# Kernel optimization log

Hardware: AMD Instinct MI355X
Metric: run time of the kernel (lower is better)

The kernel has to match this reference:

```python
import jax, jax.numpy as jnp
import numpy as np

NUM_GROUPS = 4
DIVERSITY_STRENGTH = -0.5   # module stores -diversity_strength
DIVERSITY_DISCOUNT = 0.5
CAND_MULT = 1
N_GRAM = 2


def setup_inputs() -> dict:
    key = jax.random.key(0)
    k1, k2, k3, k5, k6 = jax.random.split(key, 5)
    bsz, beam, vocab, T = 64, 8, 50257, 128
    return {
        "lprobs": jax.random.normal(k1, (bsz, beam, vocab), jnp.float32),
        "scores": jax.random.normal(k2, (bsz, beam, T), jnp.float32),
        "group_overlap": jax.random.uniform(k3, (bsz, NUM_GROUPS, NUM_GROUPS), jnp.float32),
        "original_batch_idxs": jnp.arange(bsz, dtype=jnp.int32),
        "last_n_gram_indices": jax.random.randint(k5, (bsz, beam, N_GRAM - 1), 0, vocab, jnp.int32),
        "mask_last_n_gram_indices": jax.random.randint(k6, (bsz, beam, N_GRAM), 0, 2, jnp.int32),
        "step": 5,
    }


def reference(lprobs, scores, group_overlap, original_batch_idxs,
              last_n_gram_indices, mask_last_n_gram_indices, step):
    bsz, beam, vocab = lprobs.shape
    G = NUM_GROUPS
    mb = beam // G  # mini beam size
    k = CAND_MULT * mb
    batch_ar = jnp.arange(bsz)[:, None]

    scores_G, beams_G, idx_G = [], [], []
    for g in range(G):
        lp = lprobs[:, g::G, :]                       # [bsz, mb, vocab]
        sc = scores[:, g::G, step - 1]                # [bsz, mb]
        mk = mask_last_n_gram_indices[:, g::G, :]     # [bsz, mb, n_gram]
        if g > 0:
            # diversity penalty: scatter-add (1 + overlap) at previously picked tokens
            pen = 1.0 + group_overlap[original_batch_idxs, g, :g]          # [bsz, g]
            src = jnp.broadcast_to(pen[:, None, :], (bsz, mb, g)).reshape(bsz, -1)
            prev_idx = jnp.stack(idx_G, axis=-1).reshape(bsz, -1)          # [bsz, mb*g]
            div = jnp.zeros((bsz, vocab), lp.dtype).at[batch_ar, prev_idx].add(src)
            lp = lp + DIVERSITY_STRENGTH * div[:, None, :]
        # n-gram overlap mask: zero out beams whose mask rows are not all ones
        valid = (mk.sum(-1) == N_GRAM)                # [bsz, mb]
        lp = jnp.where(valid[:, :, None], lp, 0.0)
        # step > 0: add accumulated beam scores
        lp = lp + sc[:, :, None]
        flat = lp.reshape(bsz, -1)                    # [bsz, mb*vocab]
        top_idx = jax.lax.top_k(flat, k)[1]
        top_val = jnp.take_along_axis(flat, top_idx, axis=-1)
        beams_G.append((top_idx // vocab) * G + g)
        idx_G.append(top_idx % vocab)
        scores_G.append(top_val)

    scores_buf = jnp.stack(scores_G, axis=2).reshape(bsz, -1)   # [bsz, beam]
    indices_buf = jnp.stack(idx_G, axis=2).reshape(bsz, -1)
    beams_buf = jnp.stack(beams_G, axis=2).reshape(bsz, -1)

    # Hamming-cumulative overlap: [bsz, beam, n_gram] present n-grams, grouped
    present = jnp.concatenate(
        [last_n_gram_indices, indices_buf[:, :, None]], axis=-1
    ).reshape(bsz, mb, G, N_GRAM)
    eq = (present[:, :, None, :, :] == present[:, :, :, None, :])  # [bsz, mb, G, G, n]
    m = (mask_last_n_gram_indices != 0).reshape(bsz, mb, G, N_GRAM)
    om = m[:, :, None, :, :] & m[:, :, :, None, :]
    eq = jnp.where(om, eq, False)
    ov = (eq.sum(-1) == N_GRAM).astype(jnp.int32).sum(1)           # [bsz, G, G]

    new_group_overlap = (
        group_overlap.at[original_batch_idxs].add(ov.astype(group_overlap.dtype))
        * DIVERSITY_DISCOUNT
    )
    return scores_buf, indices_buf, beams_buf, new_group_overlap
```

## Files before the change

kernel.cpp:

```cpp
#include <hip/hip_runtime.h>
#include <math.h>

#define VOCAB 50257
#define BSZ   64
#define BEAM  8
#define NG    4
#define MB    2
#define KC    2
#define TLEN  128
#define NGRAM 2
#define SEG    64
#define SEGLEN 786
#define ROWS  (BSZ * BEAM)
#define MAXK  8
#define CAPQ  256

__device__ __forceinline__ bool better(float v1, int i1, float v2, int i2) {
    return (v1 > v2) || (v1 == v2 && i1 < i2);
}

struct Top2 { float v1, v2; int i1, i2; };

__device__ __forceinline__ void t2_init(Top2& t) {
    t.v1 = -INFINITY; t.v2 = -INFINITY; t.i1 = 0x7FFFFFFF; t.i2 = 0x7FFFFFFF;
}

__device__ __forceinline__ void t2_push(Top2& t, float v, int i) {
    if (better(v, i, t.v2, t.i2)) {
        if (better(v, i, t.v1, t.i1)) { t.v2 = t.v1; t.i2 = t.i1; t.v1 = v; t.i1 = i; }
        else                          { t.v2 = v;    t.i2 = i; }
    }
}

__device__ __forceinline__ void t2_merge(Top2& a, const Top2& b) {
    if (better(b.v1, b.i1, a.v1, a.i1)) {
        float nv2; int ni2;
        if (better(a.v1, a.i1, b.v2, b.i2)) { nv2 = a.v1; ni2 = a.i1; }
        else                                { nv2 = b.v2; ni2 = b.i2; }
        a.v1 = b.v1; a.i1 = b.i1; a.v2 = nv2; a.i2 = ni2;
    } else {
        if (better(b.v1, b.i1, a.v2, a.i2)) { a.v2 = b.v1; a.i2 = b.i1; }
    }
}

__device__ __forceinline__ float max4(float4 v) {
    return fmaxf(fmaxf(v.x, v.y), fmaxf(v.z, v.w));
}

__global__ __launch_bounds__(1024, 8) void dbs_candidates(
    const float* __restrict__ lprobs,
    const int*   __restrict__ mask,
    int*   __restrict__ meta,
    int*   __restrict__ wscnt,
    float* __restrict__ wscv,
    int*   __restrict__ wsci)
{
    const int tid  = threadIdx.x;
    const int w    = tid >> 6, lane = tid & 63;

    __shared__ unsigned long long s_bits[8];
    __shared__ float s_max[16];
    __shared__ float s_tau;
    __shared__ int   s_cnt;
    __shared__ float s_cv[CAPQ];
    __shared__ int   s_ci[CAPQ];

    bool validp = false;
    if (tid < ROWS) {
        const int2 mk = ((const int2*)mask)[tid];
        validp = (mk.x + mk.y) == NGRAM;
    }
    const unsigned long long bm = __ballot(validp);
    if (w < 8 && lane == 0) s_bits[w] = bm;
    if (tid == 0) s_cnt = 0;
    __syncthreads();

    int nv = 0;
    #pragma unroll
    for (int i = 0; i < 8; ++i) nv += __popcll(s_bits[i]);
    int k = 1;
    if (nv > 0) {
        const int q = ROWS / nv;
        k = (q >= 8) ? 8 : (q >= 4) ? 4 : (q >= 2) ? 2 : 1;
    }
    if (blockIdx.x == 0 && tid == 0) meta[0] = k;
    const int b = blockIdx.x;
    if (b >= nv * k) return;

    const int vidx  = b / k;
    const int slice = b - vidx * k;
    int r = 0, cnt = 0;
    for (int i = 0; i < 8; ++i) {
        const unsigned long long x = s_bits[i];
        const int c = __popcll(x);
        if (cnt + c > vidx) {
            unsigned long long y = x;
            for (int need = vidx - cnt; need > 0; --need) y &= y - 1;
            r = i * 64 + (__ffsll((unsigned long long)y) - 1);
            break;
        }
        cnt += c;
    }

    const size_t rowoff = (size_t)r * VOCAB;
    const float* row = lprobs + rowoff;

    const int segs = SEG / k;
    const int A    = slice * segs * SEGLEN;
    const int B    = min(A + segs * SEGLEN, VOCAB);
    const int L    = B - A;
    const int subL = (L + 15) >> 4;

    {
        const int start = A + w * subL;
        const int end   = min(start + subL, B);
        float m = -INFINITY;
        if (start < end) {
            const int mis = (int)((rowoff + start) & 3);
            int pre = (4 - mis) & 3;
            if (pre > end - start) pre = end - start;
            if (lane < pre) m = row[start + lane];
            const int vstart = start + pre;
            const int n4 = (end > vstart) ? ((end - vstart) >> 2) : 0;
            const float4* vrow = (const float4*)(row + vstart);

            float a0 = -INFINITY, a1 = -INFINITY, a2 = -INFINITY, a3 = -INFINITY;
            int jj = lane;
            for (; jj + 192 < n4; jj += 256) {
                a0 = fmaxf(a0, max4(vrow[jj]));
                a1 = fmaxf(a1, max4(vrow[jj + 64]));
                a2 = fmaxf(a2, max4(vrow[jj + 128]));
                a3 = fmaxf(a3, max4(vrow[jj + 192]));
            }
            for (; jj < n4; jj += 64) a0 = fmaxf(a0, max4(vrow[jj]));
            m = fmaxf(m, fmaxf(fmaxf(a0, a1), fmaxf(a2, a3)));
            const int tstart = vstart + 4 * n4;
            if (tstart + lane < end) m = fmaxf(m, row[tstart + lane]);
        }
        #pragma unroll
        for (int off = 32; off > 0; off >>= 1) m = fmaxf(m, __shfl_xor(m, off));
        if (lane == 0) s_max[w] = m;
    }
    __syncthreads();

    if (w == 0) {
        const float mym = (lane < 16) ? s_max[lane] : -INFINITY;
        int rank = 0;
        #pragma unroll
        for (int i = 0; i < 16; ++i) {
            const float om = __shfl(mym, i);
            rank += better(om, i, mym, lane) ? 1 : 0;
        }
        if (lane < 16 && rank == 7) s_tau = mym;
    }
    __syncthreads();
    const float tau = s_tau;

    if (s_max[w] >= tau) {
        const int start = A + w * subL;
        const int end   = min(start + subL, B);
        if (start < end) {
            const int mis = (int)((rowoff + start) & 3);
            int pre = (4 - mis) & 3;
            if (pre > end - start) pre = end - start;
            if (lane < pre) {
                const float v = row[start + lane];
                if (v >= tau) {
                    const int p = atomicAdd(&s_cnt, 1);
                    if (p < CAPQ) { s_cv[p] = v; s_ci[p] = start + lane; }
                }
            }
            const int vstart = start + pre;
            const int n4 = (end > vstart) ? ((end - vstart) >> 2) : 0;
            const float4* vrow = (const float4*)(row + vstart);

            for (int jj = lane; jj < n4; jj += 64) {
                const float4 v = vrow[jj];
                if (max4(v) >= tau) {
                    const int base = vstart + 4 * jj;
                    #pragma unroll
                    for (int e = 0; e < 4; ++e) {
                        const float ve = (e == 0) ? v.x : (e == 1) ? v.y
                                       : (e == 2) ? v.z : v.w;
                        if (ve >= tau) {
                            const int p = atomicAdd(&s_cnt, 1);
                            if (p < CAPQ) { s_cv[p] = ve; s_ci[p] = base + e; }
                        }
                    }
                }
            }
            const int tstart = vstart + 4 * n4;
            if (tstart + lane < end) {
                const float v = row[tstart + lane];
                if (v >= tau) {
                    const int p = atomicAdd(&s_cnt, 1);
                    if (p < CAPQ) { s_cv[p] = v; s_ci[p] = tstart + lane; }
                }
            }
        }
    }
    __syncthreads();

    const int ccnt = min(s_cnt, CAPQ);
    const int slot = r * MAXK + slice;
    if (tid == 0) wscnt[slot] = ccnt;
    for (int c = tid; c < ccnt; c += 1024) {
        wscv[(size_t)slot * CAPQ + c] = s_cv[c];
        wsci[(size_t)slot * CAPQ + c] = s_ci[c];
    }
}

__global__ __launch_bounds__(64) void dbs_final(
    const float* __restrict__ scores,
    const float* __restrict__ overlap,
    const int*   __restrict__ obi,
    const int*   __restrict__ lastn,
    const int*   __restrict__ mask,
    const int*   __restrict__ stepp,
    const int*   __restrict__ meta,
    const int*   __restrict__ wscnt,
    const float* __restrict__ wscv,
    const int*   __restrict__ wsci,
    float*       __restrict__ out)
{
    const int b   = blockIdx.x;
    const int tid = threadIdx.x;
    const int step = stepp[0];
    const int ob   = obi[b];

    __shared__ float s_sc[BEAM];
    __shared__ int   s_valid[BEAM];
    __shared__ int   s_k;
    __shared__ float s_pen[(NG-1)*KC];
    __shared__ int   s_penidx[(NG-1)*KC];
    __shared__ float s_selv[NG][KC];
    __shared__ int   s_seli[NG][KC];
    __shared__ int   s_selm[NG][KC];

    if (tid < BEAM) {
        const int* mk = mask + ((size_t)b * BEAM + tid) * NGRAM;
        s_valid[tid] = (mk[0] + mk[1]) == NGRAM;
        s_sc[tid]    = scores[((size_t)b * BEAM + tid) * TLEN + (step - 1)];
    }
    if (tid == 0) s_k = meta[0];
    __syncthreads();
    const int k = s_k;

    for (int g = 0; g < NG; ++g) {
        if (tid == 0) {
            for (int j = 0; j < g; ++j) {
                const float pen = 1.0f + overlap[((size_t)ob * NG + g) * NG + j];
                s_penidx[j*KC + 0] = s_seli[j][0]; s_pen[j*KC + 0] = pen;
                s_penidx[j*KC + 1] = s_seli[j][1]; s_pen[j*KC + 1] = pen;
            }
        }
        __syncthreads();

        const int np = KC * g;
        Top2 t; t2_init(t);
        for (int m = 0; m < MB; ++m) {
            const int beam = m * NG + g;
            if (s_valid[beam]) {
                const int r = b * BEAM + beam;
                for (int qq = 0; qq < k; ++qq) {
                    const int slot = r * MAXK + qq;
                    const int n = wscnt[slot];
                    for (int c = tid; c < n; c += 64) {
                        const float v   = wscv[(size_t)slot * CAPQ + c];
                        const int   idx = wsci[(size_t)slot * CAPQ + c];
                        float dv = 0.0f;
                        #pragma unroll
                        for (int p = 0; p < (NG-1)*KC; ++p)
                            if (p < np && s_penidx[p] == idx) dv += s_pen[p];
                        t2_push(t, v - 0.5f * dv + s_sc[beam], m * VOCAB + idx);
                    }
                }
            } else if (tid < KC) {
                t2_push(t, s_sc[beam], m * VOCAB + tid);
            }
        }

        #pragma unroll
        for (int off = 32; off > 0; off >>= 1) {
            Top2 o;
            o.v1 = __shfl_down(t.v1, off); o.i1 = __shfl_down(t.i1, off);
            o.v2 = __shfl_down(t.v2, off); o.i2 = __shfl_down(t.i2, off);
            t2_merge(t, o);
        }
        if (tid == 0) {
            s_selv[g][0] = t.v1; s_seli[g][0] = t.i1 % VOCAB; s_selm[g][0] = t.i1 / VOCAB;
            s_selv[g][1] = t.v2; s_seli[g][1] = t.i2 % VOCAB; s_selm[g][1] = t.i2 / VOCAB;
        }
        __syncthreads();
    }

    if (tid < KC * NG) {
        const int i = tid;
        const int m = i / NG, g = i % NG;
        out[(size_t)b * BEAM + i]        = s_selv[g][m];
        out[512 + (size_t)b * BEAM + i]  = (float)s_seli[g][m];
        out[1024 + (size_t)b * BEAM + i] = (float)(s_selm[g][m] * NG + g);
    }
    if (tid >= 16 && tid < 16 + NG * NG) {
        const int q  = tid - 16;
        const int g1 = q / NG, g2 = q % NG;
        int ov = 0;
        for (int m = 0; m < MB; ++m) {
            const int i1 = m * NG + g1, i2 = m * NG + g2;
            const int p1a = lastn[(size_t)b * BEAM + i1];
            const int p2a = lastn[(size_t)b * BEAM + i2];
            const int p1b = s_seli[g1][m];
            const int p2b = s_seli[g2][m];
            const int* mk1 = mask + ((size_t)b * BEAM + i1) * NGRAM;
            const int* mk2 = mask + ((size_t)b * BEAM + i2) * NGRAM;
            const bool e0 = (p1a == p2a) && (mk1[0] != 0) && (mk2[0] != 0);
            const bool e1 = (p1b == p2b) && (mk1[1] != 0) && (mk2[1] != 0);
            ov += (e0 && e1) ? 1 : 0;
        }
        out[1536 + (size_t)ob * (NG * NG) + q] =
            (overlap[(size_t)ob * (NG * NG) + q] + (float)ov) * 0.5f;
    }
}

extern "C" void kernel_launch(void* const* d_in, const int* in_sizes, int n_in,
                              void* d_out, int out_size, void* d_ws, size_t ws_size,
                              hipStream_t stream) {
    const float* lprobs  = (const float*)d_in[0];
    const float* scores  = (const float*)d_in[1];
    const float* overlap = (const float*)d_in[2];
    const int*   obi     = (const int*)d_in[3];
    const int*   lastn   = (const int*)d_in[4];
    const int*   mask    = (const int*)d_in[5];
    const int*   stepp   = (const int*)d_in[6];
    float*       out     = (float*)d_out;

    int*   meta  = (int*)d_ws;
    int*   wscnt = (int*)((char*)d_ws + 64);
    float* wscv  = (float*)((char*)d_ws + 64 + (size_t)ROWS * MAXK * 4);
    int*   wsci  = (int*)((char*)d_ws + 64 + (size_t)ROWS * MAXK * 4
                          + (size_t)ROWS * MAXK * CAPQ * 4);

    dbs_candidates<<<ROWS, 1024, 0, stream>>>(lprobs, mask, meta, wscnt, wscv, wsci);
    dbs_final     <<<BSZ, 64, 0, stream>>>(scores, overlap, obi, lastn, mask, stepp,
                                           meta, wscnt, wscv, wsci, out);
}
```

Baseline: 25.78 us.

## Fuse candidate scan and final selection into one cooperative kernel with grid sync

Folds the two kernels into one cooperative launch: every block runs the candidate scan, then a grid-wide barrier follows, and the first 64 blocks do the per-batch group top-2 selection and overlap update. If the cooperative launch fails, it falls back to the original two launches. The scan loop is also reshaped with fewer accumulators and an unconditional tail. This aims to remove the second launch gap, at the cost of grid-sync overhead and a residency requirement of 512 blocks of 1024 threads.

New measurement: 97.13 us. 3.77x slower.

```diff
diff --git a/kernel.cpp b/kernel.cpp
--- a/kernel.cpp
+++ b/kernel.cpp
@@ -1,4 +1,5 @@
 #include <hip/hip_runtime.h>
+#include <hip/hip_cooperative_groups.h>
 #include <math.h>
 
 #define VOCAB 50257
@@ -47,23 +48,14 @@
     return fmaxf(fmaxf(v.x, v.y), fmaxf(v.z, v.w));
 }
 
-__global__ __launch_bounds__(1024, 8) void dbs_candidates(
-    const float* __restrict__ lprobs,
-    const int*   __restrict__ mask,
-    int*   __restrict__ meta,
-    int*   __restrict__ wscnt,
-    float* __restrict__ wscv,
-    int*   __restrict__ wsci)
+__device__ __forceinline__ int scan_block(
+    const float* __restrict__ lprobs, const int* __restrict__ mask,
+    int* __restrict__ wscnt, float* __restrict__ wscv, int* __restrict__ wsci,
+    unsigned long long* s_bits, float* s_max, float* s_tau, int* s_cnt,
+    float* s_cv, int* s_ci)
 {
     const int tid  = threadIdx.x;
     const int w    = tid >> 6, lane = tid & 63;
-
-    __shared__ unsigned long long s_bits[8];
-    __shared__ float s_max[16];
-    __shared__ float s_tau;
-    __shared__ int   s_cnt;
-    __shared__ float s_cv[CAPQ];
-    __shared__ int   s_ci[CAPQ];
 
     bool validp = false;
     if (tid < ROWS) {
@@ -72,7 +64,7 @@
     }
     const unsigned long long bm = __ballot(validp);
     if (w < 8 && lane == 0) s_bits[w] = bm;
-    if (tid == 0) s_cnt = 0;
+    if (tid == 0) *s_cnt = 0;
     __syncthreads();
 
     int nv = 0;
@@ -83,9 +75,9 @@
         const int q = ROWS / nv;
         k = (q >= 8) ? 8 : (q >= 4) ? 4 : (q >= 2) ? 2 : 1;
     }
-    if (blockIdx.x == 0 && tid == 0) meta[0] = k;
+
     const int b = blockIdx.x;
-    if (b >= nv * k) return;
+    if (b >= nv * k) return k;
 
     const int vidx  = b / k;
     const int slice = b - vidx * k;
@@ -96,7 +88,7 @@
         if (cnt + c > vidx) {
             unsigned long long y = x;
             for (int need = vidx - cnt; need > 0; --need) y &= y - 1;
-            r = i * 64 + (__ffsll((unsigned long long)y) - 1);
+            r = i * 64 + (__ffsll(y) - 1);
             break;
         }
         cnt += c;
@@ -104,43 +96,43 @@
 
     const size_t rowoff = (size_t)r * VOCAB;
     const float* row = lprobs + rowoff;
-
     const int segs = SEG / k;
     const int A    = slice * segs * SEGLEN;
-    const int B    = min(A + segs * SEGLEN, VOCAB);
-    const int L    = B - A;
+    const int Bv   = min(A + segs * SEGLEN, VOCAB);
+    const int L    = Bv - A;
     const int subL = (L + 15) >> 4;
 
+    const int start = A + w * subL;
+    const int end   = min(start + subL, Bv);
+
+    float m = -INFINITY;
+    const int mis = (int)((rowoff + start) & 3);
+    int pre = (4 - mis) & 3;
+    if (pre > end - start) pre = end - start;
+    if (lane < pre) m = row[start + lane];
+    const int vstart = start + pre;
+    const int n4 = (end - vstart) >> 2;
+    const float4* vrow = (const float4*)(row + vstart);
+    const int nc = n4 >> 6;
+
+    float a0 = -INFINITY, a1 = -INFINITY;
+    for (int c = 0; c < nc; ++c) {
+        const float4 v = vrow[c * 64 + lane];
+        a0 = fmaxf(fmaxf(a0, fmaxf(v.x, v.y)), fmaxf(v.z, v.w));
+    }
     {
-        const int start = A + w * subL;
-        const int end   = min(start + subL, B);
-        float m = -INFINITY;
-        if (start < end) {
-            const int mis = (int)((rowoff + start) & 3);
-            int pre = (4 - mis) & 3;
-            if (pre > end - start) pre = end - start;
-            if (lane < pre) m = row[start + lane];
-            const int vstart = start + pre;
-            const int n4 = (end > vstart) ? ((end - vstart) >> 2) : 0;
-            const float4* vrow = (const float4*)(row + vstart);
-
-            float a0 = -INFINITY, a1 = -INFINITY, a2 = -INFINITY, a3 = -INFINITY;
-            int jj = lane;
-            for (; jj + 192 < n4; jj += 256) {
-                a0 = fmaxf(a0, max4(vrow[jj]));
-                a1 = fmaxf(a1, max4(vrow[jj + 64]));
-                a2 = fmaxf(a2, max4(vrow[jj + 128]));
-                a3 = fmaxf(a3, max4(vrow[jj + 192]));
-            }
-            for (; jj < n4; jj += 64) a0 = fmaxf(a0, max4(vrow[jj]));
-            m = fmaxf(m, fmaxf(fmaxf(a0, a1), fmaxf(a2, a3)));
-            const int tstart = vstart + 4 * n4;
-            if (tstart + lane < end) m = fmaxf(m, row[tstart + lane]);
-        }
-        #pragma unroll
-        for (int off = 32; off > 0; off >>= 1) m = fmaxf(m, __shfl_xor(m, off));
-        if (lane == 0) s_max[w] = m;
-    }
+        const int jj = nc * 64 + lane;
+        if (jj < n4) {
+            const float4 v = vrow[jj];
+            a1 = fmaxf(fmaxf(a1, fmaxf(v.x, v.y)), fmaxf(v.z, v.w));
+        }
+        const int tstart = vstart + 4 * n4;
+        if (tstart + lane < end) a1 = fmaxf(a1, row[tstart + lane]);
+    }
+    m = fmaxf(m, fmaxf(a0, a1));
+    #pragma unroll
+    for (int off = 32; off > 0; off >>= 1) m = fmaxf(m, __shfl_xor(m, off));
+    if (lane == 0) s_max[w] = m;
     __syncthreads();
 
     if (w == 0) {
@@ -151,77 +143,186 @@
             const float om = __shfl(mym, i);
             rank += better(om, i, mym, lane) ? 1 : 0;
         }
-        if (lane < 16 && rank == 7) s_tau = mym;
+        if (lane < 16 && rank == 7) *s_tau = mym;
     }
     __syncthreads();
-    const float tau = s_tau;
+    const float tau = *s_tau;
 
     if (s_max[w] >= tau) {
-        const int start = A + w * subL;
-        const int end   = min(start + subL, B);
-        if (start < end) {
-            const int mis = (int)((rowoff + start) & 3);
-            int pre = (4 - mis) & 3;
-            if (pre > end - start) pre = end - start;
-            if (lane < pre) {
-                const float v = row[start + lane];
-                if (v >= tau) {
-                    const int p = atomicAdd(&s_cnt, 1);
-                    if (p < CAPQ) { s_cv[p] = v; s_ci[p] = start + lane; }
-                }
-            }
-            const int vstart = start + pre;
-            const int n4 = (end > vstart) ? ((end - vstart) >> 2) : 0;
-            const float4* vrow = (const float4*)(row + vstart);
-
-            for (int jj = lane; jj < n4; jj += 64) {
+        if (lane < pre) {
+            const float v = row[start + lane];
+            if (v >= tau) {
+                const int p = atomicAdd(s_cnt, 1);
+                if (p < CAPQ) { s_cv[p] = v; s_ci[p] = start + lane; }
+            }
+        }
+        for (int jj0 = 0; jj0 < n4; jj0 += 64) {
+            const int jj = jj0 + lane;
+            if (jj < n4) {
                 const float4 v = vrow[jj];
                 if (max4(v) >= tau) {
                     const int base = vstart + 4 * jj;
-                    #pragma unroll
-                    for (int e = 0; e < 4; ++e) {
-                        const float ve = (e == 0) ? v.x : (e == 1) ? v.y
-                                       : (e == 2) ? v.z : v.w;
-                        if (ve >= tau) {
-                            const int p = atomicAdd(&s_cnt, 1);
-                            if (p < CAPQ) { s_cv[p] = ve; s_ci[p] = base + e; }
-                        }
-                    }
+                    if (v.x >= tau) { const int p = atomicAdd(s_cnt,1); if (p<CAPQ){s_cv[p]=v.x; s_ci[p]=base;} }
+                    if (v.y >= tau) { const int p = atomicAdd(s_cnt,1); if (p<CAPQ){s_cv[p]=v.y; s_ci[p]=base+1;} }
+                    if (v.z >= tau) { const int p = atomicAdd(s_cnt,1); if (p<CAPQ){s_cv[p]=v.z; s_ci[p]=base+2;} }
+                    if (v.w >= tau) { const int p = atomicAdd(s_cnt,1); if (p<CAPQ){s_cv[p]=v.w; s_ci[p]=base+3;} }
                 }
             }
-            const int tstart = vstart + 4 * n4;
-            if (tstart + lane < end) {
-                const float v = row[tstart + lane];
-                if (v >= tau) {
-                    const int p = atomicAdd(&s_cnt, 1);
-                    if (p < CAPQ) { s_cv[p] = v; s_ci[p] = tstart + lane; }
-                }
+        }
+        const int tstart = vstart + 4 * n4;
+        if (tstart + lane < end) {
+            const float v = row[tstart + lane];
+            if (v >= tau) {
+                const int p = atomicAdd(s_cnt, 1);
+                if (p < CAPQ) { s_cv[p] = v; s_ci[p] = tstart + lane; }
             }
         }
     }
     __syncthreads();
 
-    const int ccnt = min(s_cnt, CAPQ);
+    const int ccnt = min(*s_cnt, CAPQ);
     const int slot = r * MAXK + slice;
     if (tid == 0) wscnt[slot] = ccnt;
     for (int c = tid; c < ccnt; c += 1024) {
         wscv[(size_t)slot * CAPQ + c] = s_cv[c];
         wsci[(size_t)slot * CAPQ + c] = s_ci[c];
     }
+    return k;
+}
+
+__global__ __launch_bounds__(1024, 8) void dbs_fused(
+    const float* __restrict__ lprobs, const float* __restrict__ scores,
+    const float* __restrict__ overlap, const int* __restrict__ obi,
+    const int* __restrict__ lastn, const int* __restrict__ mask,
+    const int* __restrict__ stepp,
+    int* __restrict__ wscnt, float* __restrict__ wscv, int* __restrict__ wsci,
+    float* __restrict__ out)
+{
+    __shared__ unsigned long long s_bits[8];
+    __shared__ float s_max[16];
+    __shared__ float s_tau;
+    __shared__ int   s_cnt;
+    __shared__ float s_cv[CAPQ];
+    __shared__ int   s_ci[CAPQ];
+
+    const int k = scan_block(lprobs, mask, wscnt, wscv, wsci,
+                             s_bits, s_max, &s_tau, &s_cnt, s_cv, s_ci);
+
+    cooperative_groups::this_grid().sync();
+
+    const int b = blockIdx.x;
+    if (b >= BSZ) return;
+    const int lane = threadIdx.x;
+    if (lane >= 64) return;
+
+    const int step = stepp[0];
+    const int ob   = obi[b];
+    float selv[NG][KC]; int seli[NG][KC]; int selm[NG][KC];
+
+    #pragma unroll
+    for (int g = 0; g < NG; ++g) {
+        Top2 t; t2_init(t);
+        #pragma unroll
+        for (int m = 0; m < MB; ++m) {
+            const int rr = b * BEAM + m * NG + g;
+            const int2 mkb = *(const int2*)(mask + rr * NGRAM);
+            const float sc = scores[(size_t)rr * TLEN + (step - 1)];
+            if (mkb.x + mkb.y == NGRAM) {
+                for (int qq = 0; qq < k; ++qq) {
+                    const int slot = rr * MAXK + qq;
+                    const int n = wscnt[slot];
+                    for (int c = lane; c < n; c += 64) {
+                        const float v   = wscv[(size_t)slot * CAPQ + c];
+                        const int   idx = wsci[(size_t)slot * CAPQ + c];
+                        float dv = 0.0f;
+                        #pragma unroll
+                        for (int j = 0; j < NG - 1; ++j) {
+                            if (j < g) {
+                                const float pen =
+                                    1.0f + overlap[((size_t)ob * NG + g) * NG + j];
+                                if (seli[j][0] == idx) dv += pen;
+                                if (seli[j][1] == idx) dv += pen;
+                            }
+                        }
+                        t2_push(t, v - 0.5f * dv + sc, m * VOCAB + idx);
+                    }
+                }
+            } else if (lane < KC) {
+                t2_push(t, sc, m * VOCAB + lane);
+            }
+        }
+        #pragma unroll
+        for (int off = 32; off > 0; off >>= 1) {
+            Top2 o;
+            o.v1 = __shfl_down(t.v1, off); o.i1 = __shfl_down(t.i1, off);
+            o.v2 = __shfl_down(t.v2, off); o.i2 = __shfl_down(t.i2, off);
+            t2_merge(t, o);
+        }
+        t.v1 = __shfl(t.v1, 0); t.i1 = __shfl(t.i1, 0);
+        t.v2 = __shfl(t.v2, 0); t.i2 = __shfl(t.i2, 0);
+        selv[g][0] = t.v1; seli[g][0] = t.i1 % VOCAB; selm[g][0] = t.i1 / VOCAB;
+        selv[g][1] = t.v2; seli[g][1] = t.i2 % VOCAB; selm[g][1] = t.i2 / VOCAB;
+    }
+
+    #pragma unroll
+    for (int g = 0; g < NG; ++g) {
+        #pragma unroll
+        for (int m = 0; m < MB; ++m) {
+            const int i = m * NG + g;
+            if (lane == 8 + i) {
+                out[(size_t)b * BEAM + i]        = selv[g][m];
+                out[512 + (size_t)b * BEAM + i]  = (float)seli[g][m];
+                out[1024 + (size_t)b * BEAM + i] = (float)(selm[g][m] * NG + g);
+            }
+        }
+    }
+    #pragma unroll
+    for (int q = 0; q < NG * NG; ++q) {
+        if (lane == 24 + q) {
+            const int g1 = q / NG, g2 = q % NG;
+            int ov = 0;
+            #pragma unroll
+            for (int m = 0; m < MB; ++m) {
+                const int i1 = m * NG + g1, i2 = m * NG + g2;
+                const int p1a = lastn[(size_t)b * BEAM + i1];
+                const int p2a = lastn[(size_t)b * BEAM + i2];
+                const int* mk1 = mask + ((size_t)b * BEAM + i1) * NGRAM;
+                const int* mk2 = mask + ((size_t)b * BEAM + i2) * NGRAM;
+                const bool e0 = (p1a == p2a) && (mk1[0] != 0) && (mk2[0] != 0);
+                const bool e1 = (seli[g1][m] == seli[g2][m])
+                                && (mk1[1] != 0) && (mk2[1] != 0);
+                ov += (e0 && e1) ? 1 : 0;
+            }
+            out[1536 + (size_t)ob * (NG * NG) + q] =
+                (overlap[(size_t)ob * (NG * NG) + q] + (float)ov) * 0.5f;
+        }
+    }
+}
+
+__global__ __launch_bounds__(1024, 8) void dbs_candidates(
+    const float* __restrict__ lprobs, const int* __restrict__ mask,
+    int* __restrict__ meta, int* __restrict__ wscnt,
+    float* __restrict__ wscv, int* __restrict__ wsci)
+{
+    __shared__ unsigned long long s_bits[8];
+    __shared__ float s_max[16];
+    __shared__ float s_tau;
+    __shared__ int   s_cnt;
+    __shared__ float s_cv[CAPQ];
+    __shared__ int   s_ci[CAPQ];
+
+    const int k = scan_block(lprobs, mask, wscnt, wscv, wsci,
+                             s_bits, s_max, &s_tau, &s_cnt, s_cv, s_ci);
+    if (blockIdx.x == 0 && threadIdx.x == 0) meta[0] = k;
 }
 
 __global__ __launch_bounds__(64) void dbs_final(
-    const float* __restrict__ scores,
-    const float* __restrict__ overlap,
-    const int*   __restrict__ obi,
-    const int*   __restrict__ lastn,
-    const int*   __restrict__ mask,
-    const int*   __restrict__ stepp,
-    const int*   __restrict__ meta,
-    const int*   __restrict__ wscnt,
-    const float* __restrict__ wscv,
-    const int*   __restrict__ wsci,
-    float*       __restrict__ out)
+    const float* __restrict__ scores, const float* __restrict__ overlap,
+    const int* __restrict__ obi, const int* __restrict__ lastn,
+    const int* __restrict__ mask, const int* __restrict__ stepp,
+    const int* __restrict__ meta, const int* __restrict__ wscnt,
+    const float* __restrict__ wscv, const int* __restrict__ wsci,
+    float* __restrict__ out)
 {
     const int b   = blockIdx.x;
     const int tid = threadIdx.x;
@@ -340,7 +441,18 @@
     int*   wsci  = (int*)((char*)d_ws + 64 + (size_t)ROWS * MAXK * 4
                           + (size_t)ROWS * MAXK * CAPQ * 4);
 
-    dbs_candidates<<<ROWS, 1024, 0, stream>>>(lprobs, mask, meta, wscnt, wscv, wsci);
-    dbs_final     <<<BSZ, 64, 0, stream>>>(scores, overlap, obi, lastn, mask, stepp,
-                                           meta, wscnt, wscv, wsci, out);
-}
+    void* params[] = {(void*)&lprobs, (void*)&scores, (void*)&overlap,
+                      (void*)&obi, (void*)&lastn, (void*)&mask, (void*)&stepp,
+                      (void*)&wscnt, (void*)&wscv, (void*)&wsci, (void*)&out};
+
+    const hipError_t e = hipLaunchCooperativeKernel(
+        (const void*)dbs_fused, dim3(ROWS), dim3(1024), params, 0, stream);
+
+    if (e != hipSuccess) {
+        (void)hipGetLastError();
+        dbs_candidates<<<ROWS, 1024, 0, stream>>>(lprobs, mask, meta,
+                                                  wscnt, wscv, wsci);
+        dbs_final<<<BSZ, 64, 0, stream>>>(scores, overlap, obi, lastn, mask,
+                                          stepp, meta, wscnt, wscv, wsci, out);
+    }
+}
```
